# Performance work log

Hardware: AMD Instinct MI355X
Metric: run time of the kernel (lower is better)

Reference implementation:

```python
import jax, jax.numpy as jnp
import numpy as np

B, H, S, D = 4, 16, 2048, 128


def setup_inputs() -> dict:
    key0 = jax.random.key(0)
    kq, kk, kv, km = jax.random.split(key0, 4)
    query = jax.random.normal(kq, (B, H, S, D), dtype=jnp.float32)
    key = jax.random.normal(kk, (B, H, S, D), dtype=jnp.float32)
    value = jax.random.normal(kv, (B, H, S, D), dtype=jnp.float32)
    mask = jax.random.normal(km, (1, 1, S, S), dtype=jnp.float32)
    return {"query": query, "key": key, "value": value, "mask": mask}


def reference(query, key, value, mask):
    # qk: [B, H, S, S]
    qk = jnp.einsum('bhqd,bhkd->bhqk', query, key)
    qk = qk + mask
    # NOTE: original module divides by sqrt(D) AFTER adding the mask
    scale = 1.0 / jnp.sqrt(jnp.asarray(key.shape[-1], dtype=query.dtype))
    attn = jax.nn.softmax(qk * scale, axis=-1)
    return jnp.einsum('bhqk,bhkd->bhqd', attn, value)
```

## Files before the change

### kernel.cpp

```cpp
#include <hip/hip_runtime.h>
#include <math.h>

#define SEQ   2048
#define HD    128
#define KVB   64
#define NT    (SEQ / KVB)
#define SCALE_L2E 0.12753242193263556f

typedef __bf16 bf16_t;
typedef __bf16 bf16x2 __attribute__((ext_vector_type(2)));
typedef __bf16 bf16x4 __attribute__((ext_vector_type(4)));
typedef __bf16 bf16x8 __attribute__((ext_vector_type(8)));
typedef float  f32x16 __attribute__((ext_vector_type(16)));

__device__ __forceinline__ void gl_lds16(const void* g, void* l) {
  __builtin_amdgcn_global_load_lds(
      (const __attribute__((address_space(1))) unsigned int*)g,
      (__attribute__((address_space(3))) unsigned int*)l, 16, 0, 0);
}

__global__ __launch_bounds__(256)
void prep_all(const float* __restrict__ k, const float* __restrict__ v,
              const float* __restrict__ m, char* __restrict__ kimg,
              char* __restrict__ vimg, bf16x2* __restrict__ mt2) {
  __shared__ float vtile[KVB][HD + 4];
  __shared__ float mtile[32][65];
  const int tid = threadIdx.x;
  const int bx  = blockIdx.x;

  if (bx < 2048) {
    const int bt = bx;
    const float* src = k + (size_t)bt * KVB * HD;
    char* dst = kimg + (size_t)bt * 16384;
#pragma unroll
    for (int i = 0; i < 8; ++i) {
      const int g = tid + i * 256;
      const int r = g >> 5, c4 = g & 31;
      float4 a = *(const float4*)(src + (size_t)r * HD + c4 * 4);
      const int o = (r * 256 + c4 * 8) ^ ((r & 7) << 4);
      *(bf16x4*)(dst + o) = bf16x4{(bf16_t)a.x, (bf16_t)a.y, (bf16_t)a.z, (bf16_t)a.w};
    }
  } else if (bx < 4096) {
    const int bt = bx - 2048;
    const float* src = v + (size_t)bt * KVB * HD;
    char* dst = vimg + (size_t)bt * 16384;
#pragma unroll
    for (int i = 0; i < 8; ++i) {
      const int g = tid + i * 256;
      const int r = g >> 5, c4 = g & 31;
      float4 a = *(const float4*)(src + (size_t)r * HD + c4 * 4);
      vtile[r][c4 * 4 + 0] = a.x; vtile[r][c4 * 4 + 1] = a.y;
      vtile[r][c4 * 4 + 2] = a.z; vtile[r][c4 * 4 + 3] = a.w;
    }
    __syncthreads();
#pragma unroll
    for (int i = 0; i < 8; ++i) {
      const int g = tid + i * 256;
      const int o = g * 8;
      const int d = o >> 7;
      const int inner = (o & 127) ^ ((d & 7) << 4);
      const int pe0 = inner >> 1;
      bf16x4 w;
#pragma unroll
      for (int e = 0; e < 4; ++e) {
        const int pe = pe0 + e;
        const int a  = pe >> 4;
        const int bp = pe & 15;
        const int vv = bp >> 1;
        const int sv = (vv & 1) | ((vv & 2) << 1) | ((vv & 4) >> 1);
        const int kk = a * 16 + sv * 2 + (bp & 1);
        w[e] = (bf16_t)vtile[kk][d];
      }
      *(bf16x4*)(dst + o) = w;
    }
  } else {
    const int mid = bx - 4096;
    const int k0  = (mid & 31) * 64;
    const int q0  = (mid >> 5) * 32;
#pragma unroll
    for (int i = 0; i < 2; ++i) {
      const int ix = tid + i * 256;
      const int qr = ix >> 4, c4 = ix & 15;
      float4 a = *(const float4*)(m + (size_t)(q0 + qr) * SEQ + k0 + c4 * 4);
      mtile[qr][c4 * 4 + 0] = a.x; mtile[qr][c4 * 4 + 1] = a.y;
      mtile[qr][c4 * 4 + 2] = a.z; mtile[qr][c4 * 4 + 3] = a.w;
    }
    __syncthreads();
#pragma unroll
    for (int i = 0; i < 4; ++i) {
      const int ix = tid + i * 256;
      const int kl = ix >> 5, qq = ix & 31;
      mt2[(size_t)((mid & 31) * 32 + kl) * SEQ + q0 + qq] =
          bf16x2{(bf16_t)(mtile[qq][kl] * SCALE_L2E),
                 (bf16_t)(mtile[qq][kl + 32] * SCALE_L2E)};
    }
  }
}

__global__ __launch_bounds__(256, 2)
void attn_fwd_v10(const float* __restrict__ q_g, const char* __restrict__ kimg,
                  const char* __restrict__ vimg, const bf16x2* __restrict__ mt2_g,
                  float* __restrict__ o_g) {
  __shared__ __align__(16) char ldsK[2][16384];
  __shared__ __align__(16) char ldsV[2][16384];

  const int tid  = threadIdx.x;
  const int wid  = tid >> 6;
  const int lane = tid & 63;
  const int hi   = lane >> 5;
  const int ql   = lane & 31;

  const int lin = blockIdx.x;
  const int xcd = lin & 7;
  const int idx = lin >> 3;
  const int bh  = xcd + 8 * (idx >> 4);
  const int q0  = (idx & 15) * 128;

  const float* Qb = q_g + (size_t)bh * SEQ * HD;
  float*       Ob = o_g + (size_t)bh * SEQ * HD;

  const int qrow = q0 + wid * 32 + ql;

  bf16x8 qf[8];
#pragma unroll
  for (int kd = 0; kd < 8; ++kd) {
    const float* p = Qb + (size_t)qrow * HD + kd * 16 + hi * 8;
    float4 a = *(const float4*)p;
    float4 b = *(const float4*)(p + 4);
    qf[kd] = bf16x8{(bf16_t)a.x, (bf16_t)a.y, (bf16_t)a.z, (bf16_t)a.w,
                    (bf16_t)b.x, (bf16_t)b.y, (bf16_t)b.z, (bf16_t)b.w};
  }

  f32x16 ot[4];
#pragma unroll
  for (int dt = 0; dt < 4; ++dt)
#pragma unroll
    for (int r = 0; r < 16; ++r) ot[dt][r] = 0.f;

  f32x16 lsum;
#pragma unroll
  for (int r = 0; r < 16; ++r) lsum[r] = 0.f;

#define STAGE_K(T, BUF)                                                      \
  { const char* gK = kimg + ((size_t)bh * NT + (T)) * 16384 + wid * 4096 +   \
                     lane * 16;                                              \
    char* lK = ldsK[BUF] + wid * 4096;                                       \
    _Pragma("unroll") for (int j = 0; j < 4; ++j)                            \
      gl_lds16(gK + j * 1024, lK + j * 1024); }

#define STAGE_V(T, BUF)                                                      \
  { const char* gV = vimg + ((size_t)bh * NT + (T)) * 16384 + wid * 4096 +   \
                     lane * 16;                                              \
    char* lV = ldsV[BUF] + wid * 4096;                                       \
    _Pragma("unroll") for (int j = 0; j < 4; ++j)                            \
      gl_lds16(gV + j * 1024, lV + j * 1024); }

  STAGE_K(0, 0)
  STAGE_V(0, 0)

  for (int t = 0; t < NT; ++t) {
    __syncthreads();
    const int buf = t & 1;
    const char* Kl = ldsK[buf];
    const char* Vl = ldsV[buf];
    const bool more = (t + 1 < NT);

    bf16x2 mreg[16];
    {
      const bf16x2* MTp = mt2_g + (size_t)(t * 32) * SEQ + qrow;
#pragma unroll
      for (int r = 0; r < 16; ++r) {
        const int kl = (r & 3) + 8 * (r >> 2) + 4 * hi;
        mreg[r] = MTp[(size_t)kl * SEQ];
      }
    }

    if (more) {
      STAGE_K(t + 1, buf ^ 1)
      STAGE_V(t + 1, buf ^ 1)
    }

    f32x16 s0, s1;
#pragma unroll
    for (int r = 0; r < 16; ++r) { s0[r] = 0.f; s1[r] = 0.f; }
#pragma unroll
    for (int kd = 0; kd < 8; ++kd) {
      int b0 = ql * 256 + kd * 32 + hi * 16; b0 ^= (ql & 7) << 4;
      bf16x8 kf0 = *(const bf16x8*)(Kl + b0);
      bf16x8 kf1 = *(const bf16x8*)(Kl + b0 + 8192);
      s0 = __builtin_amdgcn_mfma_f32_32x32x16_bf16(kf0, qf[kd], s0, 0, 0, 0);
      s1 = __builtin_amdgcn_mfma_f32_32x32x16_bf16(kf1, qf[kd], s1, 0, 0, 0);
    }

    float p0[16], p1[16];
#pragma unroll
    for (int r = 0; r < 16; ++r) {
      p0[r] = __builtin_amdgcn_exp2f(fmaf(s0[r], SCALE_L2E, (float)mreg[r][0]));
      p1[r] = __builtin_amdgcn_exp2f(fmaf(s1[r], SCALE_L2E, (float)mreg[r][1]));
    }
#pragma unroll
    for (int r = 0; r < 16; ++r) lsum[r] += p0[r] + p1[r];

    bf16x8 pb[2][2];
#pragma unroll
    for (int kf = 0; kf < 2; ++kf) {
      pb[0][kf] = bf16x8{(bf16_t)p0[8*kf+0], (bf16_t)p0[8*kf+1],
                         (bf16_t)p0[8*kf+2], (bf16_t)p0[8*kf+3],
                         (bf16_t)p0[8*kf+4], (bf16_t)p0[8*kf+5],
                         (bf16_t)p0[8*kf+6], (bf16_t)p0[8*kf+7]};
      pb[1][kf] = bf16x8{(bf16_t)p1[8*kf+0], (bf16_t)p1[8*kf+1],
                         (bf16_t)p1[8*kf+2], (bf16_t)p1[8*kf+3],
                         (bf16_t)p1[8*kf+4], (bf16_t)p1[8*kf+5],
                         (bf16_t)p1[8*kf+6], (bf16_t)p1[8*kf+7]};
    }

#pragma unroll
    for (int tt = 0; tt < 2; ++tt)
#pragma unroll
      for (int kf = 0; kf < 2; ++kf) {
        const int kg = tt * 2 + kf;
#pragma unroll
        for (int dt = 0; dt < 4; ++dt) {
          const int d = dt * 32 + ql;
          int byt = d * 128 + kg * 32 + hi * 16; byt ^= (d & 7) << 4;
          bf16x8 vf = *(const bf16x8*)(Vl + byt);
          ot[dt] = __builtin_amdgcn_mfma_f32_32x32x16_bf16(vf, pb[tt][kf], ot[dt], 0, 0, 0);
        }
      }
  }

  float ls[16];
#pragma unroll
  for (int r = 0; r < 16; ++r) ls[r] = lsum[r];
#pragma unroll
  for (int off = 8; off > 0; off >>= 1)
#pragma unroll
    for (int r = 0; r < off; ++r) ls[r] += ls[r + off];
  const float l_run = ls[0] + __shfl_xor(ls[0], 32, 64);

  const float rinv = 1.f / l_run;
  float* Op = Ob + (size_t)qrow * HD;
#pragma unroll
  for (int dt = 0; dt < 4; ++dt)
#pragma unroll
    for (int g2 = 0; g2 < 4; ++g2) {
      const int d = dt * 32 + 8 * g2 + 4 * hi;
      *(float4*)(Op + d) = float4{ot[dt][4*g2+0] * rinv, ot[dt][4*g2+1] * rinv,
                                  ot[dt][4*g2+2] * rinv, ot[dt][4*g2+3] * rinv};
    }
}

extern "C" void kernel_launch(void* const* d_in, const int* in_sizes, int n_in,
                              void* d_out, int out_size, void* d_ws, size_t ws_size,
                              hipStream_t stream) {
  (void)in_sizes; (void)n_in; (void)out_size; (void)ws_size;
  const float* Q = (const float*)d_in[0];
  const float* K = (const float*)d_in[1];
  const float* V = (const float*)d_in[2];
  const float* M = (const float*)d_in[3];
  float*       O = (float*)d_out;

  const size_t szImg = (size_t)64 * NT * 16384;
  char*   KI  = (char*)d_ws;
  char*   VI  = (char*)d_ws + szImg;
  bf16x2* MT2 = (bf16x2*)((char*)d_ws + 2 * szImg);

  prep_all<<<dim3(6144), 256, 0, stream>>>(K, V, M, KI, VI, MT2);
  attn_fwd_v10<<<dim3(1024), 256, 0, stream>>>(Q, KI, VI, MT2, O);
}
```

Before: 208.8 us.

## Switch attention to 16x16x32 MFMA with 8 waves per block

Replaces the 32x32x16 bf16 MFMA tiling with 16x16x32 MFMA. Each wave now owns 16 query rows, and a block runs 512 threads (8 waves) covering the same 128 queries. The V image layout permutation in the prep kernel is rewritten to match the new P-operand lane mapping. The aim is to cut per-wave register pressure (smaller accumulators) and raise occupancy and latency hiding, in exchange for more waves sharing the same LDS tiles and more, smaller MFMA issues.

```diff
diff --git a/kernel.cpp b/kernel.cpp
--- a/kernel.cpp
+++ b/kernel.cpp
@@ -11,7 +11,7 @@
 typedef __bf16 bf16x2 __attribute__((ext_vector_type(2)));
 typedef __bf16 bf16x4 __attribute__((ext_vector_type(4)));
 typedef __bf16 bf16x8 __attribute__((ext_vector_type(8)));
-typedef float  f32x16 __attribute__((ext_vector_type(16)));
+typedef float  f32x4  __attribute__((ext_vector_type(4)));
 
 __device__ __forceinline__ void gl_lds16(const void* g, void* l) {
   __builtin_amdgcn_global_load_lds(
@@ -59,16 +59,13 @@
       const int o = g * 8;
       const int d = o >> 7;
       const int inner = (o & 127) ^ ((d & 7) << 4);
-      const int pe0 = inner >> 1;
+      const int s0 = inner >> 1;
       bf16x4 w;
 #pragma unroll
       for (int e = 0; e < 4; ++e) {
-        const int pe = pe0 + e;
-        const int a  = pe >> 4;
-        const int bp = pe & 15;
-        const int vv = bp >> 1;
-        const int sv = (vv & 1) | ((vv & 2) << 1) | ((vv & 4) >> 1);
-        const int kk = a * 16 + sv * 2 + (bp & 1);
+        const int s  = s0 + e;
+        const int kk = (s & 32) | (((s >> 2) & 1) << 4) |
+                       (((s >> 3) & 3) << 2) | (s & 3);
         w[e] = (bf16_t)vtile[kk][d];
       }
       *(bf16x4*)(dst + o) = w;
@@ -97,8 +94,8 @@
   }
 }
 
-__global__ __launch_bounds__(256, 2)
-void attn_fwd_v10(const float* __restrict__ q_g, const char* __restrict__ kimg,
+__global__ __launch_bounds__(512, 4)
+void attn_fwd_v11(const float* __restrict__ q_g, const char* __restrict__ kimg,
                   const char* __restrict__ vimg, const bf16x2* __restrict__ mt2_g,
                   float* __restrict__ o_g) {
   __shared__ __align__(16) char ldsK[2][16384];
@@ -107,8 +104,8 @@
   const int tid  = threadIdx.x;
   const int wid  = tid >> 6;
   const int lane = tid & 63;
-  const int hi   = lane >> 5;
-  const int ql   = lane & 31;
+  const int hi4  = lane >> 4;
+  const int ql   = lane & 15;
 
   const int lin = blockIdx.x;
   const int xcd = lin & 7;
@@ -119,41 +116,36 @@
   const float* Qb = q_g + (size_t)bh * SEQ * HD;
   float*       Ob = o_g + (size_t)bh * SEQ * HD;
 
-  const int qrow = q0 + wid * 32 + ql;
-
-  bf16x8 qf[8];
-#pragma unroll
-  for (int kd = 0; kd < 8; ++kd) {
-    const float* p = Qb + (size_t)qrow * HD + kd * 16 + hi * 8;
+  const int qrow = q0 + wid * 16 + ql;
+
+  bf16x8 qf[4];
+#pragma unroll
+  for (int kd = 0; kd < 4; ++kd) {
+    const float* p = Qb + (size_t)qrow * HD + kd * 32 + hi4 * 8;
     float4 a = *(const float4*)p;
     float4 b = *(const float4*)(p + 4);
     qf[kd] = bf16x8{(bf16_t)a.x, (bf16_t)a.y, (bf16_t)a.z, (bf16_t)a.w,
                     (bf16_t)b.x, (bf16_t)b.y, (bf16_t)b.z, (bf16_t)b.w};
   }
 
-  f32x16 ot[4];
-#pragma unroll
-  for (int dt = 0; dt < 4; ++dt)
-#pragma unroll
-    for (int r = 0; r < 16; ++r) ot[dt][r] = 0.f;
-
-  f32x16 lsum;
-#pragma unroll
-  for (int r = 0; r < 16; ++r) lsum[r] = 0.f;
+  f32x4 ot[8];
+#pragma unroll
+  for (int dt = 0; dt < 8; ++dt) ot[dt] = f32x4{0.f, 0.f, 0.f, 0.f};
+  f32x4 lsum = f32x4{0.f, 0.f, 0.f, 0.f};
 
 #define STAGE_K(T, BUF)                                                      \
-  { const char* gK = kimg + ((size_t)bh * NT + (T)) * 16384 + wid * 4096 +   \
+  { const char* gK = kimg + ((size_t)bh * NT + (T)) * 16384 + wid * 2048 +   \
                      lane * 16;                                              \
-    char* lK = ldsK[BUF] + wid * 4096;                                       \
-    _Pragma("unroll") for (int j = 0; j < 4; ++j)                            \
-      gl_lds16(gK + j * 1024, lK + j * 1024); }
+    char* lK = ldsK[BUF] + wid * 2048;                                       \
+    gl_lds16(gK, lK);                                                        \
+    gl_lds16(gK + 1024, lK + 1024); }
 
 #define STAGE_V(T, BUF)                                                      \
-  { const char* gV = vimg + ((size_t)bh * NT + (T)) * 16384 + wid * 4096 +   \
+  { const char* gV = vimg + ((size_t)bh * NT + (T)) * 16384 + wid * 2048 +   \
                      lane * 16;                                              \
-    char* lV = ldsV[BUF] + wid * 4096;                                       \
-    _Pragma("unroll") for (int j = 0; j < 4; ++j)                            \
-      gl_lds16(gV + j * 1024, lV + j * 1024); }
+    char* lV = ldsV[BUF] + wid * 2048;                                       \
+    gl_lds16(gV, lV);                                                        \
+    gl_lds16(gV + 1024, lV + 1024); }
 
   STAGE_K(0, 0)
   STAGE_V(0, 0)
@@ -165,14 +157,14 @@
     const char* Vl = ldsV[buf];
     const bool more = (t + 1 < NT);
 
-    bf16x2 mreg[16];
+    bf16x2 mreg[8];
     {
       const bf16x2* MTp = mt2_g + (size_t)(t * 32) * SEQ + qrow;
 #pragma unroll
-      for (int r = 0; r < 16; ++r) {
-        const int kl = (r & 3) + 8 * (r >> 2) + 4 * hi;
-        mreg[r] = MTp[(size_t)kl * SEQ];
-      }
+      for (int n16 = 0; n16 < 2; ++n16)
+#pragma unroll
+        for (int r = 0; r < 4; ++r)
+          mreg[n16 * 4 + r] = MTp[(size_t)(n16 * 16 + hi4 * 4 + r) * SEQ];
     }
 
     if (more) {
@@ -180,74 +172,67 @@
       STAGE_V(t + 1, buf ^ 1)
     }
 
-    f32x16 s0, s1;
-#pragma unroll
-    for (int r = 0; r < 16; ++r) { s0[r] = 0.f; s1[r] = 0.f; }
-#pragma unroll
-    for (int kd = 0; kd < 8; ++kd) {
-      int b0 = ql * 256 + kd * 32 + hi * 16; b0 ^= (ql & 7) << 4;
-      bf16x8 kf0 = *(const bf16x8*)(Kl + b0);
-      bf16x8 kf1 = *(const bf16x8*)(Kl + b0 + 8192);
-      s0 = __builtin_amdgcn_mfma_f32_32x32x16_bf16(kf0, qf[kd], s0, 0, 0, 0);
-      s1 = __builtin_amdgcn_mfma_f32_32x32x16_bf16(kf1, qf[kd], s1, 0, 0, 0);
-    }
-
-    float p0[16], p1[16];
-#pragma unroll
-    for (int r = 0; r < 16; ++r) {
-      p0[r] = __builtin_amdgcn_exp2f(fmaf(s0[r], SCALE_L2E, (float)mreg[r][0]));
-      p1[r] = __builtin_amdgcn_exp2f(fmaf(s1[r], SCALE_L2E, (float)mreg[r][1]));
-    }
-#pragma unroll
-    for (int r = 0; r < 16; ++r) lsum[r] += p0[r] + p1[r];
-
-    bf16x8 pb[2][2];
-#pragma unroll
-    for (int kf = 0; kf < 2; ++kf) {
-      pb[0][kf] = bf16x8{(bf16_t)p0[8*kf+0], (bf16_t)p0[8*kf+1],
-                         (bf16_t)p0[8*kf+2], (bf16_t)p0[8*kf+3],
-                         (bf16_t)p0[8*kf+4], (bf16_t)p0[8*kf+5],
-                         (bf16_t)p0[8*kf+6], (bf16_t)p0[8*kf+7]};
-      pb[1][kf] = bf16x8{(bf16_t)p1[8*kf+0], (bf16_t)p1[8*kf+1],
-                         (bf16_t)p1[8*kf+2], (bf16_t)p1[8*kf+3],
-                         (bf16_t)p1[8*kf+4], (bf16_t)p1[8*kf+5],
-                         (bf16_t)p1[8*kf+6], (bf16_t)p1[8*kf+7]};
-    }
-
-#pragma unroll
-    for (int tt = 0; tt < 2; ++tt)
-#pragma unroll
-      for (int kf = 0; kf < 2; ++kf) {
-        const int kg = tt * 2 + kf;
-#pragma unroll
-        for (int dt = 0; dt < 4; ++dt) {
-          const int d = dt * 32 + ql;
-          int byt = d * 128 + kg * 32 + hi * 16; byt ^= (d & 7) << 4;
-          bf16x8 vf = *(const bf16x8*)(Vl + byt);
-          ot[dt] = __builtin_amdgcn_mfma_f32_32x32x16_bf16(vf, pb[tt][kf], ot[dt], 0, 0, 0);
-        }
-      }
-  }
-
-  float ls[16];
-#pragma unroll
-  for (int r = 0; r < 16; ++r) ls[r] = lsum[r];
-#pragma unroll
-  for (int off = 8; off > 0; off >>= 1)
-#pragma unroll
-    for (int r = 0; r < off; ++r) ls[r] += ls[r + off];
-  const float l_run = ls[0] + __shfl_xor(ls[0], 32, 64);
-
-  const float rinv = 1.f / l_run;
+    f32x4 sacc[4];
+#pragma unroll
+    for (int n = 0; n < 4; ++n) sacc[n] = f32x4{0.f, 0.f, 0.f, 0.f};
+#pragma unroll
+    for (int kd = 0; kd < 4; ++kd) {
+#pragma unroll
+      for (int n = 0; n < 4; ++n) {
+        const int row = n * 16 + ql;
+        int byt = row * 256 + (kd * 32 + hi4 * 8) * 2;
+        byt ^= (row & 7) << 4;
+        bf16x8 kf = *(const bf16x8*)(Kl + byt);
+        sacc[n] = __builtin_amdgcn_mfma_f32_16x16x32_bf16(kf, qf[kd], sacc[n], 0, 0, 0);
+      }
+    }
+
+    float p0[8], p1[8];
+#pragma unroll
+    for (int n16 = 0; n16 < 2; ++n16)
+#pragma unroll
+      for (int r = 0; r < 4; ++r) {
+        const int i = n16 * 4 + r;
+        p0[i] = __builtin_amdgcn_exp2f(
+            fmaf(sacc[n16][r], SCALE_L2E, (float)mreg[i][0]));
+        p1[i] = __builtin_amdgcn_exp2f(
+            fmaf(sacc[n16 + 2][r], SCALE_L2E, (float)mreg[i][1]));
+      }
+#pragma unroll
+    for (int r = 0; r < 4; ++r)
+      lsum[r] += (p0[r] + p0[4 + r]) + (p1[r] + p1[4 + r]);
+
+    bf16x8 pf0 = bf16x8{(bf16_t)p0[0], (bf16_t)p0[1], (bf16_t)p0[2], (bf16_t)p0[3],
+                        (bf16_t)p0[4], (bf16_t)p0[5], (bf16_t)p0[6], (bf16_t)p0[7]};
+    bf16x8 pf1 = bf16x8{(bf16_t)p1[0], (bf16_t)p1[1], (bf16_t)p1[2], (bf16_t)p1[3],
+                        (bf16_t)p1[4], (bf16_t)p1[5], (bf16_t)p1[6], (bf16_t)p1[7]};
+
+#pragma unroll
+    for (int m2 = 0; m2 < 2; ++m2) {
+      const bf16x8 pf = m2 ? pf1 : pf0;
+#pragma unroll
+      for (int dt = 0; dt < 8; ++dt) {
+        const int d = dt * 16 + ql;
+        int byt = d * 128 + (m2 * 32 + hi4 * 8) * 2;
+        byt ^= (d & 7) << 4;
+        bf16x8 vf = *(const bf16x8*)(Vl + byt);
+        ot[dt] = __builtin_amdgcn_mfma_f32_16x16x32_bf16(vf, pf, ot[dt], 0, 0, 0);
+      }
+    }
+  }
+
+  float l = (lsum[0] + lsum[1]) + (lsum[2] + lsum[3]);
+  l += __shfl_xor(l, 16, 64);
+  l += __shfl_xor(l, 32, 64);
+  const float rinv = 1.f / l;
+
   float* Op = Ob + (size_t)qrow * HD;
 #pragma unroll
-  for (int dt = 0; dt < 4; ++dt)
-#pragma unroll
-    for (int g2 = 0; g2 < 4; ++g2) {
-      const int d = dt * 32 + 8 * g2 + 4 * hi;
-      *(float4*)(Op + d) = float4{ot[dt][4*g2+0] * rinv, ot[dt][4*g2+1] * rinv,
-                                  ot[dt][4*g2+2] * rinv, ot[dt][4*g2+3] * rinv};
-    }
+  for (int dt = 0; dt < 8; ++dt) {
+    const int d = dt * 16 + hi4 * 4;
+    *(float4*)(Op + d) = float4{ot[dt][0] * rinv, ot[dt][1] * rinv,
+                                ot[dt][2] * rinv, ot[dt][3] * rinv};
+  }
 }
 
 extern "C" void kernel_launch(void* const* d_in, const int* in_sizes, int n_in,
@@ -266,5 +251,5 @@
   bf16x2* MT2 = (bf16x2*)((char*)d_ws + 2 * szImg);
 
   prep_all<<<dim3(6144), 256, 0, stream>>>(K, V, M, KI, VI, MT2);
-  attn_fwd_v10<<<dim3(1024), 256, 0, stream>>>(Q, KI, VI, MT2, O);
-}
+  attn_fwd_v11<<<dim3(1024), 512, 0, stream>>>(Q, KI, VI, MT2, O);
+}
```

Result: no change. 212.3 us (+1.7%).

## Single-buffer K tile, split KV tile into halves, raise occupancy to 3 blocks

Applied to the files above, without the earlier changes.

K is now single-buffered in LDS, and each KV tile is processed in two 32-key halves so only one score accumulator is live at a time. An extra barrier mid-tile lets the next K tile load once the second half's QK is done. The row-sum accumulator shrinks from 16 lanes to 4. Together these cut LDS from 64KB to 48KB and reduce register pressure, which targets 3 blocks per CU instead of 2. The cost is an added barrier per tile and less overlap of the K prefetch with compute.

```diff
diff --git a/kernel.cpp b/kernel.cpp
--- a/kernel.cpp
+++ b/kernel.cpp
@@ -11,6 +11,7 @@
 typedef __bf16 bf16x2 __attribute__((ext_vector_type(2)));
 typedef __bf16 bf16x4 __attribute__((ext_vector_type(4)));
 typedef __bf16 bf16x8 __attribute__((ext_vector_type(8)));
+typedef float  f32x4  __attribute__((ext_vector_type(4)));
 typedef float  f32x16 __attribute__((ext_vector_type(16)));
 
 __device__ __forceinline__ void gl_lds16(const void* g, void* l) {
@@ -97,11 +98,11 @@
   }
 }
 
-__global__ __launch_bounds__(256, 2)
-void attn_fwd_v10(const float* __restrict__ q_g, const char* __restrict__ kimg,
+__global__ __launch_bounds__(256, 3)
+void attn_fwd_v12(const float* __restrict__ q_g, const char* __restrict__ kimg,
                   const char* __restrict__ vimg, const bf16x2* __restrict__ mt2_g,
                   float* __restrict__ o_g) {
-  __shared__ __align__(16) char ldsK[2][16384];
+  __shared__ __align__(16) char ldsK[16384];
   __shared__ __align__(16) char ldsV[2][16384];
 
   const int tid  = threadIdx.x;
@@ -137,14 +138,12 @@
 #pragma unroll
     for (int r = 0; r < 16; ++r) ot[dt][r] = 0.f;
 
-  f32x16 lsum;
-#pragma unroll
-  for (int r = 0; r < 16; ++r) lsum[r] = 0.f;
-
-#define STAGE_K(T, BUF)                                                      \
+  f32x4 lsum = f32x4{0.f, 0.f, 0.f, 0.f};
+
+#define STAGE_K(T)                                                           \
   { const char* gK = kimg + ((size_t)bh * NT + (T)) * 16384 + wid * 4096 +   \
                      lane * 16;                                              \
-    char* lK = ldsK[BUF] + wid * 4096;                                       \
+    char* lK = ldsK + wid * 4096;                                            \
     _Pragma("unroll") for (int j = 0; j < 4; ++j)                            \
       gl_lds16(gK + j * 1024, lK + j * 1024); }
 
@@ -155,14 +154,49 @@
     _Pragma("unroll") for (int j = 0; j < 4; ++j)                            \
       gl_lds16(gV + j * 1024, lV + j * 1024); }
 
-  STAGE_K(0, 0)
+#define HALF(H)                                                              \
+  {                                                                          \
+    f32x16 s;                                                                \
+    _Pragma("unroll") for (int r = 0; r < 16; ++r) s[r] = 0.f;               \
+    _Pragma("unroll") for (int kd = 0; kd < 8; ++kd) {                       \
+      int b0 = ql * 256 + kd * 32 + hi * 16; b0 ^= (ql & 7) << 4;            \
+      bf16x8 kf = *(const bf16x8*)(ldsK + b0 + (H) * 8192);                  \
+      s = __builtin_amdgcn_mfma_f32_32x32x16_bf16(kf, qf[kd], s, 0, 0, 0);   \
+    }                                                                        \
+    if (H == 1) {                                                            \
+      __syncthreads();                      \
+      if (more) { STAGE_K(t + 1) }          \
+    }                                                                        \
+    float p[16];                                                             \
+    _Pragma("unroll") for (int r = 0; r < 16; ++r)                           \
+      p[r] = __builtin_amdgcn_exp2f(                                         \
+          fmaf(s[r], SCALE_L2E, (float)mreg[r][H]));                         \
+    _Pragma("unroll") for (int r = 0; r < 16; ++r) lsum[r & 3] += p[r];      \
+    bf16x8 pb[2];                                                            \
+    _Pragma("unroll") for (int kf2 = 0; kf2 < 2; ++kf2)                      \
+      pb[kf2] = bf16x8{(bf16_t)p[8*kf2+0], (bf16_t)p[8*kf2+1],               \
+                       (bf16_t)p[8*kf2+2], (bf16_t)p[8*kf2+3],               \
+                       (bf16_t)p[8*kf2+4], (bf16_t)p[8*kf2+5],               \
+                       (bf16_t)p[8*kf2+6], (bf16_t)p[8*kf2+7]};              \
+    _Pragma("unroll") for (int kf2 = 0; kf2 < 2; ++kf2) {                    \
+      const int kg = (H) * 2 + kf2;                                          \
+      _Pragma("unroll") for (int dt = 0; dt < 4; ++dt) {                     \
+        const int d = dt * 32 + ql;                                          \
+        int byt = d * 128 + kg * 32 + hi * 16; byt ^= (d & 7) << 4;          \
+        bf16x8 vf = *(const bf16x8*)(Vl + byt);                              \
+        ot[dt] = __builtin_amdgcn_mfma_f32_32x32x16_bf16(vf, pb[kf2],        \
+                                                         ot[dt], 0, 0, 0);   \
+      }                                                                      \
+    }                                                                        \
+  }
+
+  STAGE_K(0)
   STAGE_V(0, 0)
 
   for (int t = 0; t < NT; ++t) {
     __syncthreads();
-    const int buf = t & 1;
-    const char* Kl = ldsK[buf];
-    const char* Vl = ldsV[buf];
+    const int vbuf = t & 1;
+    const char* Vl = ldsV[vbuf];
     const bool more = (t + 1 < NT);
 
     bf16x2 mreg[16];
@@ -175,70 +209,16 @@
       }
     }
 
-    if (more) {
-      STAGE_K(t + 1, buf ^ 1)
-      STAGE_V(t + 1, buf ^ 1)
-    }
-
-    f32x16 s0, s1;
-#pragma unroll
-    for (int r = 0; r < 16; ++r) { s0[r] = 0.f; s1[r] = 0.f; }
-#pragma unroll
-    for (int kd = 0; kd < 8; ++kd) {
-      int b0 = ql * 256 + kd * 32 + hi * 16; b0 ^= (ql & 7) << 4;
-      bf16x8 kf0 = *(const bf16x8*)(Kl + b0);
-      bf16x8 kf1 = *(const bf16x8*)(Kl + b0 + 8192);
-      s0 = __builtin_amdgcn_mfma_f32_32x32x16_bf16(kf0, qf[kd], s0, 0, 0, 0);
-      s1 = __builtin_amdgcn_mfma_f32_32x32x16_bf16(kf1, qf[kd], s1, 0, 0, 0);
-    }
-
-    float p0[16], p1[16];
-#pragma unroll
-    for (int r = 0; r < 16; ++r) {
-      p0[r] = __builtin_amdgcn_exp2f(fmaf(s0[r], SCALE_L2E, (float)mreg[r][0]));
-      p1[r] = __builtin_amdgcn_exp2f(fmaf(s1[r], SCALE_L2E, (float)mreg[r][1]));
-    }
-#pragma unroll
-    for (int r = 0; r < 16; ++r) lsum[r] += p0[r] + p1[r];
-
-    bf16x8 pb[2][2];
-#pragma unroll
-    for (int kf = 0; kf < 2; ++kf) {
-      pb[0][kf] = bf16x8{(bf16_t)p0[8*kf+0], (bf16_t)p0[8*kf+1],
-                         (bf16_t)p0[8*kf+2], (bf16_t)p0[8*kf+3],
-                         (bf16_t)p0[8*kf+4], (bf16_t)p0[8*kf+5],
-                         (bf16_t)p0[8*kf+6], (bf16_t)p0[8*kf+7]};
-      pb[1][kf] = bf16x8{(bf16_t)p1[8*kf+0], (bf16_t)p1[8*kf+1],
-                         (bf16_t)p1[8*kf+2], (bf16_t)p1[8*kf+3],
-                         (bf16_t)p1[8*kf+4], (bf16_t)p1[8*kf+5],
-                         (bf16_t)p1[8*kf+6], (bf16_t)p1[8*kf+7]};
-    }
-
-#pragma unroll
-    for (int tt = 0; tt < 2; ++tt)
-#pragma unroll
-      for (int kf = 0; kf < 2; ++kf) {
-        const int kg = tt * 2 + kf;
-#pragma unroll
-        for (int dt = 0; dt < 4; ++dt) {
-          const int d = dt * 32 + ql;
-          int byt = d * 128 + kg * 32 + hi * 16; byt ^= (d & 7) << 4;
-          bf16x8 vf = *(const bf16x8*)(Vl + byt);
-          ot[dt] = __builtin_amdgcn_mfma_f32_32x32x16_bf16(vf, pb[tt][kf], ot[dt], 0, 0, 0);
-        }
-      }
-  }
-
-  float ls[16];
-#pragma unroll
-  for (int r = 0; r < 16; ++r) ls[r] = lsum[r];
-#pragma unroll
-  for (int off = 8; off > 0; off >>= 1)
-#pragma unroll
-    for (int r = 0; r < off; ++r) ls[r] += ls[r + off];
-  const float l_run = ls[0] + __shfl_xor(ls[0], 32, 64);
-
-  const float rinv = 1.f / l_run;
+    if (more) { STAGE_V(t + 1, vbuf ^ 1) }
+
+    HALF(0)
+    HALF(1)
+  }
+
+  float l = (lsum[0] + lsum[1]) + (lsum[2] + lsum[3]);
+  l += __shfl_xor(l, 32, 64);
+  const float rinv = 1.f / l;
+
   float* Op = Ob + (size_t)qrow * HD;
 #pragma unroll
   for (int dt = 0; dt < 4; ++dt)
@@ -266,5 +246,5 @@
   bf16x2* MT2 = (bf16x2*)((char*)d_ws + 2 * szImg);
 
   prep_all<<<dim3(6144), 256, 0, stream>>>(K, V, M, KI, VI, MT2);
-  attn_fwd_v10<<<dim3(1024), 256, 0, stream>>>(Q, KI, VI, MT2, O);
-}
+  attn_fwd_v12<<<dim3(1024), 256, 0, stream>>>(Q, KI, VI, MT2, O);
+}
```

After: 434.2 us. 2.08x slower.
